# Optimization experiments

Hardware: AMD Instinct MI355X
Metric: run time of the kernel (lower is better)

The kernel has to match this reference:

```python
import jax, jax.numpy as jnp
import numpy as np

D, P, MC = 512, 256, 128   # state dim, obs dim, control dim
H, M, T = 32, 64, 1024     # num filters, Hankel/filter length, horizon
GAMMA = 0.9


def setup_inputs() -> dict:
    rng = np.random.default_rng(0)
    # Stable dynamics: scale spectral radius to 0.95
    A = rng.standard_normal((D, D)).astype(np.float32)
    A *= np.float32(0.95 / np.max(np.abs(np.linalg.eigvals(A))))
    B = (rng.standard_normal((D, MC)) / np.sqrt(D)).astype(np.float32)
    C = (rng.standard_normal((P, D)) / np.sqrt(D)).astype(np.float32)
    # SPD cost matrices
    Q_obs = np.eye(P, dtype=np.float32)
    R = (0.1 * np.eye(MC)).astype(np.float32)
    # LQR-like feedback gain (small, applied to y_obs as in the source)
    K = (0.02 * rng.standard_normal((MC, P))).astype(np.float32)
    # Spectral filters from Hankel matrix: Z_ij = gamma^(i+j+2) * 2/((i+j+2)^3-(i+j+2))
    idx = np.arange(M)
    ij = idx[:, None] + idx[None, :] + 2
    Z = (GAMMA ** ij) * 2.0 / (ij ** 3 - ij)
    w, V = np.linalg.eigh(Z)
    sigma = np.abs(w[-H:])
    phi = V[:, -H:]
    sigma_phi = (sigma ** 0.25)[:, None] * phi.T        # [H, M]
    sigma_phi_M = sigma_phi.astype(np.float32)
    # sum over the inner l-loop of sigma_phi_m (the source sums contributions over l)
    s_m = sigma_phi.sum(axis=1).astype(np.float32)       # [H]
    # Learned controller tensor M_il -> [m_control, H, h, p]
    M_tensor = (0.01 * rng.standard_normal((MC, H, H, P))).astype(np.float32)
    x0 = rng.standard_normal(D).astype(np.float32)
    return {
        "A": jnp.asarray(A), "B": jnp.asarray(B), "C": jnp.asarray(C),
        "Q_obs": jnp.asarray(Q_obs), "R": jnp.asarray(R), "K": jnp.asarray(K),
        "M_tensor": jnp.asarray(M_tensor),
        "sigma_phi_M": jnp.asarray(sigma_phi_M), "s_m": jnp.asarray(s_m),
        "x0": jnp.asarray(x0),
    }


def reference(A, B, C, Q_obs, R, K, M_tensor, sigma_phi_M, s_m, x0):
    h, m = sigma_phi_M.shape          # filters, history window
    mc = B.shape[1]
    p = C.shape[0]

    # CAB[i] = C @ A^i @ B for i = 0..h  (Markov parameters for y_nat)
    def pow_step(Ap, _):
        return Ap @ A, C @ (Ap @ B)
    _, CAB = jax.lax.scan(pow_step, jnp.eye(A.shape[0], dtype=A.dtype), None, length=h + 1)  # [h+1, p, mc]

    # Pre-contract M_tensor with the inner filter weights (sum over j/l):
    # u_pert[c] = sum_{i,k,p'} M2[c,i,p'] * sigma_phi_M[i,k] * y_nat_{t-k}[p']
    M2 = jnp.einsum('cijq,j->ciq', M_tensor, s_m)  # [mc, h, p]

    def step(carry, _):
        x, u_buf, y_buf = carry            # x:[d], u_buf:[h+1,mc] newest-first, y_buf:[m,p] newest-first
        y_obs = C @ x                      # [p]
        # natural observation: strip effect of past controls
        y_nat = y_obs - jnp.einsum('ipc,ic->p', CAB, u_buf)
        y_buf = jnp.concatenate([y_nat[None, :], y_buf[:-1]], axis=0)
        # spectral projection of y_nat history, then contract with learned tensor
        y_proj = sigma_phi_M @ y_buf       # [h, p]
        u_pert = jnp.einsum('ciq,iq->c', M2, y_proj)  # [mc]
        u = -(K @ y_obs) + u_pert
        cost = y_obs @ (Q_obs @ y_obs) + u @ (R @ u)
        u_buf = jnp.concatenate([u[None, :], u_buf[:-1]], axis=0)
        x = A @ x + B @ u
        return (x, u_buf, y_buf), cost

    init = (x0,
            jnp.zeros((h + 1, mc), dtype=x0.dtype),
            jnp.zeros((m, p), dtype=x0.dtype))
    _, costs = jax.lax.scan(step, init, None, length=T)
    return costs  # [T] per-step losses
```

## Files before the change

kernel.cpp:

```cpp
#include <hip/hip_runtime.h>

#define TPB 256
#define NWG 214
#define MAXJ 48

__device__ __forceinline__ void cst(float* p, float v) {
  __hip_atomic_store(p, v, __ATOMIC_RELAXED, __HIP_MEMORY_SCOPE_AGENT);
}
__device__ __forceinline__ void cstu(unsigned* p, unsigned v) {
  __hip_atomic_store(p, v, __ATOMIC_RELAXED, __HIP_MEMORY_SCOPE_AGENT);
}
__device__ __forceinline__ float cld(const float* p) {
  return __hip_atomic_load(p, __ATOMIC_RELAXED, __HIP_MEMORY_SCOPE_AGENT);
}
__device__ __forceinline__ float2 cld2(const float* p) {
  unsigned long long u = __hip_atomic_load(
      reinterpret_cast<const unsigned long long*>(p), __ATOMIC_RELAXED,
      __HIP_MEMORY_SCOPE_AGENT);
  float2 v;
  __builtin_memcpy(&v, &u, 8);
  return v;
}

__device__ __forceinline__ void grid_barrier(unsigned* __restrict__ arr,
                                             int bid, int tid, unsigned phase) {
  asm volatile("s_waitcnt vmcnt(0)" ::: "memory");
  __syncthreads();
  if (tid == 0)
    __hip_atomic_store(arr + (bid << 5), phase, __ATOMIC_RELAXED,
                       __HIP_MEMORY_SCOPE_AGENT);
  if (tid < NWG) {
    while (__hip_atomic_load(arr + (tid << 5), __ATOMIC_RELAXED,
                             __HIP_MEMORY_SCOPE_AGENT) < phase)
      __builtin_amdgcn_s_sleep(1);
  }
  __atomic_signal_fence(__ATOMIC_SEQ_CST);
  __syncthreads();
}

__device__ void gemm_tile(const float* __restrict__ X, const float* __restrict__ Y,
                          float* __restrict__ Z, int M, int N, int Kd,
                          int mtile, int ntile) {
  __shared__ float Xs[16][65];
  __shared__ float Ys[16][65];
  const int tx = threadIdx.x & 15;
  const int ty = threadIdx.x >> 4;
  const int mbase = mtile * 64;
  const int nbase = ntile * 64;
  float acc[4][4] = {};
  for (int k0 = 0; k0 < Kd; k0 += 16) {
#pragma unroll
    for (int r = 0; r < 4; ++r) {
      int idx = threadIdx.x + 256 * r;
      int mm = idx >> 4, kk = idx & 15;
      int gm = mbase + mm, gk = k0 + kk;
      Xs[kk][mm] = (gm < M && gk < Kd) ? X[(size_t)gm * Kd + gk] : 0.f;
      int nn = idx & 63, k2 = idx >> 6;
      int gn = nbase + nn, gk2 = k0 + k2;
      Ys[k2][nn] = (gk2 < Kd && gn < N) ? Y[(size_t)gk2 * N + gn] : 0.f;
    }
    __syncthreads();
#pragma unroll
    for (int kk = 0; kk < 16; ++kk) {
      float xv[4], yv[4];
#pragma unroll
      for (int a = 0; a < 4; ++a) xv[a] = Xs[kk][ty * 4 + a];
#pragma unroll
      for (int b = 0; b < 4; ++b) yv[b] = Ys[kk][tx * 4 + b];
#pragma unroll
      for (int a = 0; a < 4; ++a)
#pragma unroll
        for (int b = 0; b < 4; ++b) acc[a][b] += xv[a] * yv[b];
    }
    __syncthreads();
  }
#pragma unroll
  for (int a = 0; a < 4; ++a) {
    int gm = mbase + ty * 4 + a;
    if (gm < M) {
#pragma unroll
      for (int b = 0; b < 4; ++b) {
        int gn = nbase + tx * 4 + b;
        if (gn < N) Z[(size_t)gm * N + gn] = acc[a][b];
      }
    }
  }
}

struct JobBatch {
  int n;
  int start[MAXJ + 1];
  int xsel[MAXJ], xoff[MAXJ], ysel[MAXJ], yoff[MAXJ], zoff[MAXJ];
  int M[MAXJ], N[MAXJ], K[MAXJ];
};

__global__ __launch_bounds__(256) void multi_gemm(JobBatch jb,
    const float* __restrict__ A, const float* __restrict__ Bm,
    const float* __restrict__ C, const float* __restrict__ Km,
    float* __restrict__ ws) {
  int b = blockIdx.x;
  int j = 0;
  while (j < jb.n - 1 && b >= jb.start[j + 1]) ++j;
  int rel = b - jb.start[j];
  const float* bases[5] = {ws, A, Bm, C, Km};
  const float* X = bases[jb.xsel[j]] + jb.xoff[j];
  const float* Y = bases[jb.ysel[j]] + jb.yoff[j];
  float* Z = ws + jb.zoff[j];
  int tn = jb.N[j] >> 6;
  gemm_tile(X, Y, Z, jb.M[j], jb.N[j], jb.K[j], rel / tn, rel % tn);
}

__global__ __launch_bounds__(256) void m2_kernel(const float* __restrict__ MT,
    const float* __restrict__ sm, float* __restrict__ M2g) {
  int idx = blockIdx.x * 256 + threadIdx.x;
  if (idx >= 128 * 32 * 256) return;
  int q = idx & 255;
  int ci = idx >> 8;
  const float* base = MT + (size_t)ci * 32 * 256 + q;
  float acc = 0.f;
#pragma unroll
  for (int j = 0; j < 32; ++j) acc += base[j * 256] * sm[j];
  M2g[idx] = acc;
}

__global__ __launch_bounds__(256) void wfir_kernel(const float* __restrict__ M2g,
    const float* __restrict__ Phi, float* __restrict__ W) {
  int idx = blockIdx.x * 256 + threadIdx.x;
  if (idx >= 64 * 32768) return;
  int j = idx >> 15;
  int cq = idx & 32767;
  int c = cq >> 8;
  int q = cq & 255;
  float acc = 0.f;
#pragma unroll
  for (int i = 0; i < 32; ++i)
    acc = fmaf(Phi[(i << 6) | j], M2g[(size_t)(((c << 5) | i) << 8) | q], acc);
  W[idx] = acc;
}

__global__ __launch_bounds__(256) void axpy_acl(const float* __restrict__ A,
    const float* __restrict__ BKC, float* __restrict__ Acl, float* __restrict__ P1) {
  int i = blockIdx.x * 256 + threadIdx.x;
  if (i < 262144) {
    float v = A[i] - BKC[i];
    Acl[i] = v;
    P1[i] = v;
  }
}

__global__ void init_kernel(const float* __restrict__ x0, float* __restrict__ xh,
    float* __restrict__ eh, float* __restrict__ ynh, float* __restrict__ uh0,
    float* __restrict__ dbnd, unsigned* __restrict__ arr) {
  int i = blockIdx.x * 256 + threadIdx.x;
  int stride = gridDim.x * 256;
  for (int k = i; k < 524288; k += stride) cst(xh + k, 0.f);
  for (int k = i; k < 139264; k += stride) cst(eh + k, 0.f);
  for (int k = i; k < 262144; k += stride) cst(ynh + k, 0.f);
  for (int k = i; k < 8192; k += stride) cst(uh0 + k, 0.f);
  for (int k = i; k < NWG * 32; k += stride) cstu(arr + k, 0u);
  if (i < 512) cst(dbnd + i, x0[i]);
}

__global__ __launch_bounds__(TPB, 1) void main_kernel(
    const float* __restrict__ B, const float* __restrict__ C,
    const float* __restrict__ x0, const float* __restrict__ Wfir,
    const float* __restrict__ KC, const float* __restrict__ W0C,
    const float* __restrict__ Pp, const float* __restrict__ CAp,
    const float* __restrict__ W0CAp, const float* __restrict__ Rnp,
    const float* __restrict__ AB33p, const float* __restrict__ CAB33p,
    const float* __restrict__ W0CAB33p, const float* __restrict__ A8k,
    float* __restrict__ xh, float* __restrict__ uh0, float* __restrict__ eh,
    float* __restrict__ ynh, float* __restrict__ dbnd,
    unsigned* __restrict__ arr) {
  __shared__ float smA[64 * 256];
  __shared__ float smY[8 * 256];
  __shared__ float smV[512];
  __shared__ float smW[8 * 128];
  __shared__ float smVx[8 * 516];
  __shared__ float redsc[4][16];
  const int bid = blockIdx.x;
  const int tid = threadIdx.x;

  if (bid < 128) {
    for (int i = tid; i < 16384; i += TPB) {
      int j = i >> 8;
      smA[i] = (j >= 1) ? Wfir[(size_t)j * 32768 + bid * 256 + (i & 255)] : 0.f;
    }
  }
  __syncthreads();

#pragma unroll 1
  for (int ph = 0; ph <= 130; ++ph) {
    const int T = ph * 8;

    if (bid < 128) {
      if (ph >= 1 && ph < 129) {
        const int Ty = T - 8;
        const int c = bid;
        for (int i2 = tid; i2 < 1024; i2 += TPB) {
          float2 v = cld2(ynh + (size_t)Ty * 256 + 2 * i2);
          smY[2 * i2] = v.x;
          smY[2 * i2 + 1] = v.y;
        }
        __syncthreads();
        const int q = tid;
        float yreg[8];
#pragma unroll
        for (int s = 0; s < 8; ++s) yreg[s] = smY[s * 256 + q];
        const int wv = tid >> 6;
        const int lane = tid & 63;
#pragma unroll
        for (int kt = 0; kt < 5; ++kt) {
          const int r0 = 1 + 16 * kt;
          float wreg[23];
#pragma unroll
          for (int i = 0; i < 23; ++i) {
            const int j = r0 - 7 + i;
            wreg[i] = (j >= 1 && j <= 63) ? smA[j * 256 + q] : 0.f;
          }
          float acc[16];
#pragma unroll
          for (int a = 0; a < 16; ++a) acc[a] = 0.f;
#pragma unroll
          for (int a = 0; a < 16; ++a)
#pragma unroll
            for (int s = 0; s < 8; ++s) acc[a] += wreg[a + 7 - s] * yreg[s];
#pragma unroll
          for (int a = 0; a < 16; ++a) {
            float v = acc[a];
            v += __shfl_xor(v, 32);
            v += __shfl_xor(v, 16);
            v += __shfl_xor(v, 8);
            v += __shfl_xor(v, 4);
            v += __shfl_xor(v, 2);
            v += __shfl_xor(v, 1);
            if (lane == 0) redsc[wv][a] = v;
          }
          __syncthreads();
          if (tid < 16) {
            const int r = r0 + tid;
            if (r <= 70) {
              float sum = redsc[0][tid] + redsc[1][tid] + redsc[2][tid] + redsc[3][tid];
              atomicAdd(&eh[(size_t)(Ty + r) * 128 + c], sum);
            }
          }
          __syncthreads();
        }
      }
    } else if (bid < 144) {
      if (ph < 128) {
        const int r = bid - 128;
        const int s = r >> 1;
        const int half = (r & 1) << 7;
        {
          float2 v = cld2(dbnd + (size_t)ph * 512 + 2 * tid);
          smV[2 * tid] = v.x;
          smV[2 * tid + 1] = v.y;
        }
        __syncthreads();
        const float* Mrow = (s == 0) ? C : (CAp + (size_t)(s - 1) * 131072);
        const int row = half + (tid >> 1);
        const int seg = tid & 1;
        const float4* m4 = (const float4*)(Mrow + (size_t)row * 512 + seg * 256);
        const float4* v4 = (const float4*)(smV + seg * 256);
        float a = 0.f;
#pragma unroll
        for (int it = 0; it < 64; ++it) {
          float4 mm = m4[it], vv = v4[it];
          a += mm.x * vv.x + mm.y * vv.y + mm.z * vv.z + mm.w * vv.w;
        }
        a += __shfl_down(a, 1);
        if (seg == 0) atomicAdd(&ynh[(size_t)(T + s) * 256 + row], a);
        __syncthreads();
      }
    } else if (bid < 151) {
      if (ph < 128) {
        const int m = bid - 144;
        for (int i2 = tid; i2 < 512; i2 += TPB) {
          float2 v = cld2(uh0 + (size_t)(64 + T - 33) * 128 + 2 * i2);
          smW[2 * i2] = v.x;
          smW[2 * i2 + 1] = v.y;
        }
        __syncthreads();
        const int row = tid;
        const float4* m4 = (const float4*)(CAB33p + (size_t)m * 32768 + (size_t)row * 128);
        for (int s = m + 1; s < 8; ++s) {
          const float4* u4 = (const float4*)(smW + (s - m - 1) * 128);
          float a = 0.f;
#pragma unroll
          for (int it = 0; it < 32; ++it) {
            float4 mm = m4[it], vv = u4[it];
            a += mm.x * vv.x + mm.y * vv.y + mm.z * vv.z + mm.w * vv.w;
          }
          atomicAdd(&ynh[(size_t)(T + s) * 256 + row], a);
        }
        __syncthreads();
      }
    } else if (bid < 159) {
      if (ph < 128) {
        const int s = bid - 151;
        {
          float2 v = cld2(dbnd + (size_t)ph * 512 + 2 * tid);
          smV[2 * tid] = v.x;
          smV[2 * tid + 1] = v.y;
        }
        __syncthreads();
        const float* Mrow = (s == 0) ? W0C : (W0CAp + (size_t)(s - 1) * 65536);
        const int row = tid >> 1;
        const int seg = tid & 1;
        const float4* m4 = (const float4*)(Mrow + (size_t)row * 512 + seg * 256);
        const float4* v4 = (const float4*)(smV + seg * 256);
        float a = 0.f;
#pragma unroll
        for (int it = 0; it < 64; ++it) {
          float4 mm = m4[it], vv = v4[it];
          a += mm.x * vv.x + mm.y * vv.y + mm.z * vv.z + mm.w * vv.w;
        }
        a += __shfl_down(a, 1);
        if (seg == 0) atomicAdd(&eh[(size_t)(T + s) * 128 + row], a);
        __syncthreads();
      }
    } else if (bid < 166) {
      if (ph < 128) {
        const int m = bid - 159;
        for (int i2 = tid; i2 < 512; i2 += TPB) {
          float2 v = cld2(uh0 + (size_t)(64 + T - 33) * 128 + 2 * i2);
          smW[2 * i2] = v.x;
          smW[2 * i2 + 1] = v.y;
        }
        __syncthreads();
        const int row = tid >> 1;
        const int seg = tid & 1;
        const float4* m4 = (const float4*)(W0CAB33p + (size_t)m * 16384 + (size_t)row * 128 + seg * 64);
        for (int s = m + 1; s < 8; ++s) {
          const float4* u4 = (const float4*)(smW + (s - m - 1) * 128 + seg * 64);
          float a = 0.f;
#pragma unroll
          for (int it = 0; it < 16; ++it) {
            float4 mm = m4[it], vv = u4[it];
            a += mm.x * vv.x + mm.y * vv.y + mm.z * vv.z + mm.w * vv.w;
          }
          a += __shfl_down(a, 1);
          if (seg == 0) atomicAdd(&eh[(size_t)(T + s) * 128 + row], a);
        }
        __syncthreads();
      }
    } else if (bid < 174) {
      if (ph < 127) {
        const int g = bid - 166;
        {
          float2 v = cld2(dbnd + (size_t)ph * 512 + 2 * tid);
          smV[2 * tid] = v.x;
          smV[2 * tid + 1] = v.y;
        }
        for (int i2 = tid; i2 < 512; i2 += TPB) {
          float2 v = cld2(uh0 + (size_t)(64 + T - 33) * 128 + 2 * i2);
          smW[2 * i2] = v.x;
          smW[2 * i2 + 1] = v.y;
        }
        __syncthreads();
        const int row = g * 64 + (tid >> 2);
        const int l4 = tid & 3;
        float a = 0.f;
        {
          const float4* m4 = (const float4*)(A8k + (size_t)row * 512 + l4 * 128);
          const float4* v4 = (const float4*)(smV + l4 * 128);
#pragma unroll
          for (int it = 0; it < 32; ++it) {
            float4 mm = m4[it], vv = v4[it];
            a += mm.x * vv.x + mm.y * vv.y + mm.z * vv.z + mm.w * vv.w;
          }
        }
#pragma unroll
        for (int m = 0; m < 8; ++m) {
          const float4* m4 = (const float4*)(AB33p + (size_t)m * 65536 + (size_t)row * 128 + l4 * 32);
          const float4* v4 = (const float4*)(smW + (7 - m) * 128 + l4 * 32);
#pragma unroll
          for (int it = 0; it < 8; ++it) {
            float4 mm = m4[it], vv = v4[it];
            a += mm.x * vv.x + mm.y * vv.y + mm.z * vv.z + mm.w * vv.w;
          }
        }
        a += __shfl_down(a, 2);
        a += __shfl_down(a, 1);
        if (l4 == 0) cst(&dbnd[(size_t)(ph + 1) * 512 + row], a);
        __syncthreads();
      }
    } else if (bid < 190) {
      if (ph >= 2 && ph < 130) {
        const int Tq = T - 16;
        const int r = bid - 174;
        const int s = r >> 1;
        const int half = (r & 1) << 8;
        {
          const float* src = (ph == 2) ? x0 : (xh + (size_t)(Tq - 1) * 512);
          float2 v = cld2(src + 2 * tid);
          smV[2 * tid] = v.x;
          smV[2 * tid + 1] = v.y;
        }
        __syncthreads();
        const int pslot = (ph == 2) ? s : (s + 1);
        const int row = half + tid;
        if (pslot == 0) {
          atomicAdd(&xh[(size_t)Tq * 512 + row], smV[row]);
        } else {
          const float4* m4 = (const float4*)(Pp + (size_t)(pslot - 1) * 262144 + (size_t)row * 512);
          const float4* v4 = (const float4*)smV;
          float a = 0.f;
#pragma unroll 8
          for (int it = 0; it < 128; ++it) {
            float4 mm = m4[it], vv = v4[it];
            a += mm.x * vv.x + mm.y * vv.y + mm.z * vv.z + mm.w * vv.w;
          }
          atomicAdd(&xh[(size_t)(Tq + s) * 512 + row], a);
        }
        __syncthreads();
      }
    } else if (bid < 206) {
      if (ph >= 2 && ph < 130) {
        const int Tq = T - 16;
        const int r = bid - 190;
        const int i = r >> 1;
        const int half = (r & 1) << 8;
        for (int i2 = tid; i2 < 512; i2 += TPB) {
          int idx = 2 * i2;
          float2 v;
          if (ph == 2 && idx < 128) {
            v.x = 0.f;
            v.y = 0.f;
          } else {
            v = cld2(eh + (size_t)(Tq - 1) * 128 + idx);
          }
          smW[idx] = v.x;
          smW[idx + 1] = v.y;
        }
        __syncthreads();
        const int row = half + tid;
        const float* Rrow = (i == 0) ? (B + (size_t)row * 128)
                                     : (Rnp + (size_t)(i - 1) * 65536 + (size_t)row * 128);
        const float4* m4 = (const float4*)Rrow;
        for (int s = i; s < 8; ++s) {
          const float4* e4 = (const float4*)(smW + (s - i) * 128);
          float a = 0.f;
#pragma unroll
          for (int it = 0; it < 32; ++it) {
            float4 mm = m4[it], vv = e4[it];
            a += mm.x * vv.x + mm.y * vv.y + mm.z * vv.z + mm.w * vv.w;
          }
          atomicAdd(&xh[(size_t)(Tq + s) * 512 + row], a);
        }
        __syncthreads();
      }
    } else {
      if (ph >= 3 && ph < 131) {
        const int Tu = T - 24;
        const int g = bid - 206;
        for (int i2 = tid; i2 < 2048; i2 += TPB) {
          int idx = 2 * i2;
          int rr = idx >> 9;
          int cc = idx & 511;
          float2 v = cld2(xh + (size_t)(Tu + rr) * 512 + cc);
          smVx[rr * 516 + cc] = v.x;
          smVx[rr * 516 + cc + 1] = v.y;
        }
        __syncthreads();
        const int o = tid >> 1;
        const int par = tid & 1;
        const int s = o >> 4;
        const int lr = o & 15;
        const int row = g * 16 + lr;
        const float4* m4 = (const float4*)(KC + (size_t)row * 512 + par * 256);
        const float4* v4 = (const float4*)(smVx + s * 516 + par * 256);
        float a = 0.f;
#pragma unroll
        for (int it = 0; it < 64; ++it) {
          float4 mm = m4[it], vv = v4[it];
          a += mm.x * vv.x + mm.y * vv.y + mm.z * vv.z + mm.w * vv.w;
        }
        a += __shfl_down(a, 1);
        if (par == 0) {
          float u = cld(&eh[(size_t)(Tu + s) * 128 + row]) - a;
          cst(&uh0[(size_t)(64 + Tu + s) * 128 + row], u);
        }
        __syncthreads();
      }
    }

    grid_barrier(arr, bid, tid, (unsigned)(ph + 1));
  }
}

__global__ __launch_bounds__(256) void cost_kernel(const float* __restrict__ C,
    const float* __restrict__ Q, const float* __restrict__ R,
    const float* __restrict__ xh, const float* __restrict__ uh0,
    float* __restrict__ out) {
  __shared__ float xs[512];
  __shared__ float ys[256];
  __shared__ float us[128];
  __shared__ float redw[4];
  const int t = blockIdx.x;
  const int tid = threadIdx.x;
  {
    float2 v = cld2(xh + (size_t)t * 512 + 2 * tid);
    xs[2 * tid] = v.x;
    xs[2 * tid + 1] = v.y;
  }
  if (tid < 64) {
    float2 v = cld2(uh0 + (size_t)(64 + t) * 128 + 2 * tid);
    us[2 * tid] = v.x;
    us[2 * tid + 1] = v.y;
  }
  __syncthreads();
  {
    const float4* m4 = (const float4*)(C + (size_t)tid * 512);
    const float4* v4 = (const float4*)xs;
    float a = 0.f;
    for (int it = 0; it < 128; ++it) {
      float4 mm = m4[it], vv = v4[it];
      a += mm.x * vv.x + mm.y * vv.y + mm.z * vv.z + mm.w * vv.w;
    }
    ys[tid] = a;
  }
  __syncthreads();
  float acc;
  {
    const float* Qr = Q + (size_t)tid * 256;
    float qy = 0.f;
    for (int k = 0; k < 256; ++k) qy = fmaf(Qr[k], ys[k], qy);
    acc = qy * ys[tid];
  }
  if (tid < 128) {
    const float* Rr = R + (size_t)tid * 128;
    float ru = 0.f;
    for (int k = 0; k < 128; ++k) ru = fmaf(Rr[k], us[k], ru);
    acc += ru * us[tid];
  }
  float v = acc;
  v += __shfl_xor(v, 32);
  v += __shfl_xor(v, 16);
  v += __shfl_xor(v, 8);
  v += __shfl_xor(v, 4);
  v += __shfl_xor(v, 2);
  v += __shfl_xor(v, 1);
  if ((tid & 63) == 0) redw[tid >> 6] = v;
  __syncthreads();
  if (tid == 0) out[t] = redw[0] + redw[1] + redw[2] + redw[3];
}

extern "C" void kernel_launch(void* const* d_in, const int* in_sizes, int n_in,
                              void* d_out, int out_size, void* d_ws, size_t ws_size,
                              hipStream_t stream) {
  (void)in_sizes; (void)n_in; (void)out_size; (void)ws_size;
  const float* A = (const float*)d_in[0];
  const float* B = (const float*)d_in[1];
  const float* C = (const float*)d_in[2];
  const float* Q = (const float*)d_in[3];
  const float* R = (const float*)d_in[4];
  const float* Km = (const float*)d_in[5];
  const float* MT = (const float*)d_in[6];
  const float* Phi = (const float*)d_in[7];
  const float* sm = (const float*)d_in[8];
  const float* x0 = (const float*)d_in[9];

  float* ws = (float*)d_ws;
  const int oWfir = 0;
  const int oKC = 2097152;
  const int oW0C = 2162688;
  const int oAcl = 2228224;
  const int oP = 2490368;
  const int oCA = 4587520;
  const int oW0CA = 5505024;
  const int oRn = 5963776;
  const int oApB = 6422528;
  const int oAB33 = 6946816;
  const int oCAB33 = 7471104;
  const int oW0CAB33 = 7700480;
  const int oA2 = 7815168;
  const int oA4 = 8077312;
  const int oA8 = 8339456;
  const int oA16 = 8601600;
  const int oA32 = 8863744;
  const int oM2 = 9125888;
  const int oBKC = oM2;
  const int oxh = 10174464;
  const int ouh0 = 10698752;
  const int oeh = 10838016;
  const int oynh = 10977280;
  const int odbnd = 11239424;
  const int oarr = 11306496;

  float* xh = ws + oxh;
  float* uh0 = ws + ouh0;
  float* eh = ws + oeh;
  float* ynh = ws + oynh;
  float* dbnd = ws + odbnd;
  unsigned* arr = (unsigned*)(ws + oarr);

  JobBatch jb;
  jb.n = 0;
  jb.start[0] = 0;
  auto J = [&](int xs_, int xo, int ys_, int yo, int zo, int M, int N, int K) {
    int i = jb.n++;
    jb.xsel[i] = xs_; jb.xoff[i] = xo; jb.ysel[i] = ys_; jb.yoff[i] = yo;
    jb.zoff[i] = zo; jb.M[i] = M; jb.N[i] = N; jb.K[i] = K;
    jb.start[i + 1] = jb.start[i] + (M >> 6) * (N >> 6);
  };
  auto L = [&]() {
    multi_gemm<<<dim3(jb.start[jb.n]), dim3(256), 0, stream>>>(jb, A, B, C, Km, ws);
    jb.n = 0;
    jb.start[0] = 0;
  };

  init_kernel<<<dim3(2048), dim3(256), 0, stream>>>(x0, xh, eh, ynh, uh0, dbnd, arr);
  m2_kernel<<<dim3(4096), dim3(256), 0, stream>>>(MT, sm, ws + oM2);
  wfir_kernel<<<dim3(8192), dim3(256), 0, stream>>>(ws + oM2, Phi, ws + oWfir);

  J(4, 0, 3, 0, oKC, 128, 512, 256);
  J(1, 0, 1, 0, oA2, 512, 512, 512);
  J(1, 0, 2, 0, oApB, 512, 128, 512);
  J(3, 0, 1, 0, oCA, 256, 512, 512);
  L();
  J(2, 0, 0, oKC, oBKC, 512, 512, 128);
  J(0, oA2, 0, oA2, oA4, 512, 512, 512);
  J(0, oCA, 1, 0, oCA + 131072, 256, 512, 512);
  J(1, 0, 0, oApB, oApB + 65536, 512, 128, 512);
  J(0, oWfir, 3, 0, oW0C, 128, 512, 256);
  L();
  axpy_acl<<<dim3(1024), dim3(256), 0, stream>>>(A, ws + oBKC, ws + oAcl, ws + oP);
  J(0, oA4, 0, oA4, oA8, 512, 512, 512);
  J(0, oP, 0, oP, oP + 262144, 512, 512, 512);
  J(0, oCA, 0, oA2, oCA + 2 * 131072, 256, 512, 512);
  J(0, oCA + 131072, 0, oA2, oCA + 3 * 131072, 256, 512, 512);
  J(0, oW0C, 1, 0, oW0CA, 128, 512, 512);
  J(0, oW0C, 0, oA2, oW0CA + 65536, 128, 512, 512);
  J(0, oA2, 0, oApB, oApB + 2 * 65536, 512, 128, 512);
  J(0, oA2, 0, oApB + 65536, oApB + 3 * 65536, 512, 128, 512);
  L();
  J(0, oA8, 0, oA8, oA16, 512, 512, 512);
  J(0, oP, 0, oP + 262144, oP + 2 * 262144, 512, 512, 512);
  J(0, oP + 262144, 0, oP + 262144, oP + 3 * 262144, 512, 512, 512);
  for (int i = 1; i <= 3; ++i)
    J(0, oCA + (i - 1) * 131072, 0, oA4, oCA + (i + 3) * 131072, 256, 512, 512);
  for (int i = 1; i <= 2; ++i)
    J(0, oW0CA + (i - 1) * 65536, 0, oA2, oW0CA + (i + 1) * 65536, 128, 512, 512);
  for (int k = 1; k <= 4; ++k)
    J(0, oA4, 0, oApB + (k - 1) * 65536, oApB + (k + 3) * 65536, 512, 128, 512);
  J(0, oP, 2, 0, oRn, 512, 128, 512);
  J(0, oP + 262144, 2, 0, oRn + 65536, 512, 128, 512);
  L();
  J(0, oA16, 0, oA16, oA32, 512, 512, 512);
  for (int i = 1; i <= 4; ++i)
    J(0, oP + (i - 1) * 262144, 0, oP + 3 * 262144, oP + (i + 3) * 262144, 512, 512, 512);
  for (int i = 1; i <= 3; ++i)
    J(0, oW0CA + (i - 1) * 65536, 0, oA4, oW0CA + (i + 3) * 65536, 128, 512, 512);
  J(0, oP + 2 * 262144, 2, 0, oRn + 2 * 65536, 512, 128, 512);
  J(0, oP + 3 * 262144, 2, 0, oRn + 3 * 65536, 512, 128, 512);
  L();
  for (int m = 0; m <= 7; ++m)
    J(0, oA32, 0, oApB + m * 65536, oAB33 + m * 65536, 512, 128, 512);
  for (int i = 5; i <= 7; ++i)
    J(0, oP + (i - 1) * 262144, 2, 0, oRn + (i - 1) * 65536, 512, 128, 512);
  L();
  for (int m = 0; m <= 6; ++m)
    J(3, 0, 0, oAB33 + m * 65536, oCAB33 + m * 32768, 256, 128, 512);
  for (int m = 0; m <= 6; ++m)
    J(0, oW0C, 0, oAB33 + m * 65536, oW0CAB33 + m * 16384, 128, 128, 512);
  L();

  main_kernel<<<dim3(NWG), dim3(TPB), 0, stream>>>(
      B, C, x0, ws + oWfir, ws + oKC, ws + oW0C, ws + oP, ws + oCA,
      ws + oW0CA, ws + oRn, ws + oAB33, ws + oCAB33, ws + oW0CAB33,
      ws + oA8, xh, uh0, eh, ynh, dbnd, arr);

  cost_kernel<<<dim3(1024), dim3(256), 0, stream>>>(C, Q, R, xh, uh0,
                                                    (float*)d_out);
}
```

Measured before the change: 3.325 ms.

## Use hierarchical grid barrier and spread dense matvec roles over more workgroups

Replaces the flat grid barrier, where every workgroup polled all flags, with a two-level barrier: 8 group leaders each poll about 30 workgroup flags and publish a group flag, and all workgroups then poll only the 8 group flags. It also doubles the workgroups for the x-propagation (A^8 plus AB33) and the P-power x-reconstruction roles. Each workgroup now covers fewer rows, with split dot products joined by shuffles, which shortens the per-phase critical path. The grid grows from 214 to 238 persistent workgroups, and the barrier gains an extra hop of latency in exchange for less polling traffic.

```diff
diff --git a/kernel.cpp b/kernel.cpp
--- a/kernel.cpp
+++ b/kernel.cpp
@@ -1,14 +1,29 @@
 #include <hip/hip_runtime.h>
 
 #define TPB 256
-#define NWG 214
 #define MAXJ 48
+
+#define SC_N 128
+#define YD0 128
+#define YU0 144
+#define WD0 151
+#define WU0 159
+#define DT0 166
+#define XP0 182
+#define XR0 214
+#define U0 230
+#define NWG 238
+#define NGRP 8
+#define GCH 30
 
 __device__ __forceinline__ void cst(float* p, float v) {
   __hip_atomic_store(p, v, __ATOMIC_RELAXED, __HIP_MEMORY_SCOPE_AGENT);
 }
 __device__ __forceinline__ void cstu(unsigned* p, unsigned v) {
   __hip_atomic_store(p, v, __ATOMIC_RELAXED, __HIP_MEMORY_SCOPE_AGENT);
+}
+__device__ __forceinline__ unsigned cldu(const unsigned* p) {
+  return __hip_atomic_load(p, __ATOMIC_RELAXED, __HIP_MEMORY_SCOPE_AGENT);
 }
 __device__ __forceinline__ float cld(const float* p) {
   return __hip_atomic_load(p, __ATOMIC_RELAXED, __HIP_MEMORY_SCOPE_AGENT);
@@ -23,16 +38,22 @@
 }
 
 __device__ __forceinline__ void grid_barrier(unsigned* __restrict__ arr,
+                                             unsigned* __restrict__ grp,
                                              int bid, int tid, unsigned phase) {
   asm volatile("s_waitcnt vmcnt(0)" ::: "memory");
   __syncthreads();
-  if (tid == 0)
-    __hip_atomic_store(arr + (bid << 5), phase, __ATOMIC_RELAXED,
-                       __HIP_MEMORY_SCOPE_AGENT);
-  if (tid < NWG) {
-    while (__hip_atomic_load(arr + (tid << 5), __ATOMIC_RELAXED,
-                             __HIP_MEMORY_SCOPE_AGENT) < phase)
-      __builtin_amdgcn_s_sleep(1);
+  if (tid == 0) cstu(arr + (bid << 5), phase);
+  if (bid < NGRP) {
+    const int lo = bid * GCH;
+    const int n = (NWG - lo < GCH) ? (NWG - lo) : GCH;
+    if (tid < n) {
+      while (cldu(arr + ((lo + tid) << 5)) < phase) __builtin_amdgcn_s_sleep(1);
+    }
+    __syncthreads();
+    if (tid == 0) cstu(grp + (bid << 5), phase);
+  }
+  if (tid < NGRP) {
+    while (cldu(grp + (tid << 5)) < phase) __builtin_amdgcn_s_sleep(1);
   }
   __atomic_signal_fence(__ATOMIC_SEQ_CST);
   __syncthreads();
@@ -150,7 +171,8 @@
 
 __global__ void init_kernel(const float* __restrict__ x0, float* __restrict__ xh,
     float* __restrict__ eh, float* __restrict__ ynh, float* __restrict__ uh0,
-    float* __restrict__ dbnd, unsigned* __restrict__ arr) {
+    float* __restrict__ dbnd, unsigned* __restrict__ arr,
+    unsigned* __restrict__ grp) {
   int i = blockIdx.x * 256 + threadIdx.x;
   int stride = gridDim.x * 256;
   for (int k = i; k < 524288; k += stride) cst(xh + k, 0.f);
@@ -158,6 +180,7 @@
   for (int k = i; k < 262144; k += stride) cst(ynh + k, 0.f);
   for (int k = i; k < 8192; k += stride) cst(uh0 + k, 0.f);
   for (int k = i; k < NWG * 32; k += stride) cstu(arr + k, 0u);
+  for (int k = i; k < NGRP * 32; k += stride) cstu(grp + k, 0u);
   if (i < 512) cst(dbnd + i, x0[i]);
 }
 
@@ -171,7 +194,7 @@
     const float* __restrict__ W0CAB33p, const float* __restrict__ A8k,
     float* __restrict__ xh, float* __restrict__ uh0, float* __restrict__ eh,
     float* __restrict__ ynh, float* __restrict__ dbnd,
-    unsigned* __restrict__ arr) {
+    unsigned* __restrict__ arr, unsigned* __restrict__ grp) {
   __shared__ float smA[64 * 256];
   __shared__ float smY[8 * 256];
   __shared__ float smV[512];
@@ -181,7 +204,7 @@
   const int bid = blockIdx.x;
   const int tid = threadIdx.x;
 
-  if (bid < 128) {
+  if (bid < SC_N) {
     for (int i = tid; i < 16384; i += TPB) {
       int j = i >> 8;
       smA[i] = (j >= 1) ? Wfir[(size_t)j * 32768 + bid * 256 + (i & 255)] : 0.f;
@@ -193,7 +216,7 @@
   for (int ph = 0; ph <= 130; ++ph) {
     const int T = ph * 8;
 
-    if (bid < 128) {
+    if (bid < SC_N) {
       if (ph >= 1 && ph < 129) {
         const int Ty = T - 8;
         const int c = bid;
@@ -247,9 +270,9 @@
           __syncthreads();
         }
       }
-    } else if (bid < 144) {
+    } else if (bid < YU0) {
       if (ph < 128) {
-        const int r = bid - 128;
+        const int r = bid - YD0;
         const int s = r >> 1;
         const int half = (r & 1) << 7;
         {
@@ -273,9 +296,9 @@
         if (seg == 0) atomicAdd(&ynh[(size_t)(T + s) * 256 + row], a);
         __syncthreads();
       }
-    } else if (bid < 151) {
+    } else if (bid < WD0) {
       if (ph < 128) {
-        const int m = bid - 144;
+        const int m = bid - YU0;
         for (int i2 = tid; i2 < 512; i2 += TPB) {
           float2 v = cld2(uh0 + (size_t)(64 + T - 33) * 128 + 2 * i2);
           smW[2 * i2] = v.x;
@@ -296,9 +319,9 @@
         }
         __syncthreads();
       }
-    } else if (bid < 159) {
+    } else if (bid < WU0) {
       if (ph < 128) {
-        const int s = bid - 151;
+        const int s = bid - WD0;
         {
           float2 v = cld2(dbnd + (size_t)ph * 512 + 2 * tid);
           smV[2 * tid] = v.x;
@@ -320,9 +343,9 @@
         if (seg == 0) atomicAdd(&eh[(size_t)(T + s) * 128 + row], a);
         __syncthreads();
       }
-    } else if (bid < 166) {
+    } else if (bid < DT0) {
       if (ph < 128) {
-        const int m = bid - 159;
+        const int m = bid - WU0;
         for (int i2 = tid; i2 < 512; i2 += TPB) {
           float2 v = cld2(uh0 + (size_t)(64 + T - 33) * 128 + 2 * i2);
           smW[2 * i2] = v.x;
@@ -345,9 +368,9 @@
         }
         __syncthreads();
       }
-    } else if (bid < 174) {
+    } else if (bid < XP0) {
       if (ph < 127) {
-        const int g = bid - 166;
+        const int g = bid - DT0;
         {
           float2 v = cld2(dbnd + (size_t)ph * 512 + 2 * tid);
           smV[2 * tid] = v.x;
@@ -359,39 +382,40 @@
           smW[2 * i2 + 1] = v.y;
         }
         __syncthreads();
-        const int row = g * 64 + (tid >> 2);
-        const int l4 = tid & 3;
+        const int row = g * 32 + (tid >> 3);
+        const int l4 = tid & 7;
         float a = 0.f;
         {
-          const float4* m4 = (const float4*)(A8k + (size_t)row * 512 + l4 * 128);
-          const float4* v4 = (const float4*)(smV + l4 * 128);
-#pragma unroll
-          for (int it = 0; it < 32; ++it) {
+          const float4* m4 = (const float4*)(A8k + (size_t)row * 512 + l4 * 64);
+          const float4* v4 = (const float4*)(smV + l4 * 64);
+#pragma unroll
+          for (int it = 0; it < 16; ++it) {
             float4 mm = m4[it], vv = v4[it];
             a += mm.x * vv.x + mm.y * vv.y + mm.z * vv.z + mm.w * vv.w;
           }
         }
 #pragma unroll
         for (int m = 0; m < 8; ++m) {
-          const float4* m4 = (const float4*)(AB33p + (size_t)m * 65536 + (size_t)row * 128 + l4 * 32);
-          const float4* v4 = (const float4*)(smW + (7 - m) * 128 + l4 * 32);
-#pragma unroll
-          for (int it = 0; it < 8; ++it) {
+          const float4* m4 = (const float4*)(AB33p + (size_t)m * 65536 + (size_t)row * 128 + l4 * 16);
+          const float4* v4 = (const float4*)(smW + (7 - m) * 128 + l4 * 16);
+#pragma unroll
+          for (int it = 0; it < 4; ++it) {
             float4 mm = m4[it], vv = v4[it];
             a += mm.x * vv.x + mm.y * vv.y + mm.z * vv.z + mm.w * vv.w;
           }
         }
+        a += __shfl_down(a, 4);
         a += __shfl_down(a, 2);
         a += __shfl_down(a, 1);
         if (l4 == 0) cst(&dbnd[(size_t)(ph + 1) * 512 + row], a);
         __syncthreads();
       }
-    } else if (bid < 190) {
+    } else if (bid < XR0) {
       if (ph >= 2 && ph < 130) {
         const int Tq = T - 16;
-        const int r = bid - 174;
-        const int s = r >> 1;
-        const int half = (r & 1) << 8;
+        const int r = bid - XP0;
+        const int s = r >> 2;
+        const int qtr = (r & 3) << 7;
         {
           const float* src = (ph == 2) ? x0 : (xh + (size_t)(Tq - 1) * 512);
           float2 v = cld2(src + 2 * tid);
@@ -400,26 +424,29 @@
         }
         __syncthreads();
         const int pslot = (ph == 2) ? s : (s + 1);
-        const int row = half + tid;
+        const int row = qtr + (tid >> 1);
+        const int seg = tid & 1;
         if (pslot == 0) {
-          atomicAdd(&xh[(size_t)Tq * 512 + row], smV[row]);
+          if (seg == 0) atomicAdd(&xh[(size_t)Tq * 512 + row], smV[row]);
         } else {
-          const float4* m4 = (const float4*)(Pp + (size_t)(pslot - 1) * 262144 + (size_t)row * 512);
-          const float4* v4 = (const float4*)smV;
+          const float4* m4 = (const float4*)(Pp + (size_t)(pslot - 1) * 262144 +
+                                             (size_t)row * 512 + seg * 256);
+          const float4* v4 = (const float4*)(smV + seg * 256);
           float a = 0.f;
-#pragma unroll 8
-          for (int it = 0; it < 128; ++it) {
+#pragma unroll
+          for (int it = 0; it < 64; ++it) {
             float4 mm = m4[it], vv = v4[it];
             a += mm.x * vv.x + mm.y * vv.y + mm.z * vv.z + mm.w * vv.w;
           }
-          atomicAdd(&xh[(size_t)(Tq + s) * 512 + row], a);
-        }
-        __syncthreads();
-      }
-    } else if (bid < 206) {
+          a += __shfl_down(a, 1);
+          if (seg == 0) atomicAdd(&xh[(size_t)(Tq + s) * 512 + row], a);
+        }
+        __syncthreads();
+      }
+    } else if (bid < U0) {
       if (ph >= 2 && ph < 130) {
         const int Tq = T - 16;
-        const int r = bid - 190;
+        const int r = bid - XR0;
         const int i = r >> 1;
         const int half = (r & 1) << 8;
         for (int i2 = tid; i2 < 512; i2 += TPB) {
@@ -452,9 +479,9 @@
         __syncthreads();
       }
     } else {
-      if (ph >= 3 && ph < 131) {
+      if (ph >= 3) {
         const int Tu = T - 24;
-        const int g = bid - 206;
+        const int g = bid - U0;
         for (int i2 = tid; i2 < 2048; i2 += TPB) {
           int idx = 2 * i2;
           int rr = idx >> 9;
@@ -486,7 +513,7 @@
       }
     }
 
-    grid_barrier(arr, bid, tid, (unsigned)(ph + 1));
+    grid_barrier(arr, grp, bid, tid, (unsigned)(ph + 1));
   }
 }
 
@@ -588,6 +615,7 @@
   const int oynh = 10977280;
   const int odbnd = 11239424;
   const int oarr = 11306496;
+  const int ogrp = oarr + NWG * 32;
 
   float* xh = ws + oxh;
   float* uh0 = ws + ouh0;
@@ -595,6 +623,7 @@
   float* ynh = ws + oynh;
   float* dbnd = ws + odbnd;
   unsigned* arr = (unsigned*)(ws + oarr);
+  unsigned* grp = (unsigned*)(ws + ogrp);
 
   JobBatch jb;
   jb.n = 0;
@@ -611,7 +640,8 @@
     jb.start[0] = 0;
   };
 
-  init_kernel<<<dim3(2048), dim3(256), 0, stream>>>(x0, xh, eh, ynh, uh0, dbnd, arr);
+  init_kernel<<<dim3(2048), dim3(256), 0, stream>>>(x0, xh, eh, ynh, uh0, dbnd,
+                                                    arr, grp);
   m2_kernel<<<dim3(4096), dim3(256), 0, stream>>>(MT, sm, ws + oM2);
   wfir_kernel<<<dim3(8192), dim3(256), 0, stream>>>(ws + oM2, Phi, ws + oWfir);
 
@@ -670,7 +700,7 @@
   main_kernel<<<dim3(NWG), dim3(TPB), 0, stream>>>(
       B, C, x0, ws + oWfir, ws + oKC, ws + oW0C, ws + oP, ws + oCA,
       ws + oW0CA, ws + oRn, ws + oAB33, ws + oCAB33, ws + oW0CAB33,
-      ws + oA8, xh, uh0, eh, ynh, dbnd, arr);
+      ws + oA8, xh, uh0, eh, ynh, dbnd, arr, grp);
 
   cost_kernel<<<dim3(1024), dim3(256), 0, stream>>>(C, Q, R, xh, uh0,
                                                     (float*)d_out);
```

Measured after the change: 3.371 ms. No clear change (+1.4%).
